# Kernel tuning notes

Measured on AMD Instinct MI355X. Metric: run time of the kernel, lower is better.

## Reference

```python
import jax, jax.numpy as jnp
import numpy as np

N, E = 20000, 320000
IN, HID, HEADS, OUT = 512, 128, 2, 64


def setup_inputs() -> dict:
    key = jax.random.key(0)
    ks = jax.random.split(key, 16)
    g = lambda k, shape, fan: jax.random.normal(k, shape, jnp.float32) * np.float32(1.0 / np.sqrt(fan))
    HC = HEADS * HID
    return {
        "x": jax.random.normal(ks[0], (N, IN), jnp.float32),
        "edge_index": jax.random.randint(ks[1], (2, E), 0, N, dtype=jnp.int32),
        "edge_attr": jax.random.uniform(ks[2], (E, 1), jnp.float32),
        # GATv2Conv 1: lin_l, lin_r (both biased), lin_edge (no bias), att [H,C], out bias [H*C]
        "W1l": g(ks[3], (IN, HC), IN), "b1l": jnp.zeros((HC,), jnp.float32),
        "W1r": g(ks[4], (IN, HC), IN), "b1r": jnp.zeros((HC,), jnp.float32),
        "W1e": g(ks[5], (1, HC), 1), "att1": g(ks[6], (HEADS, HID), HID),
        "bias1": jnp.zeros((HC,), jnp.float32),
        # GATv2Conv 2: heads=1
        "W2l": g(ks[7], (HC, OUT), HC), "b2l": jnp.zeros((OUT,), jnp.float32),
        "W2r": g(ks[8], (HC, OUT), HC), "b2r": jnp.zeros((OUT,), jnp.float32),
        "W2e": g(ks[9], (1, OUT), 1), "att2": g(ks[10], (1, OUT), OUT),
        "bias2": jnp.zeros((OUT,), jnp.float32),
    }


def _gatv2(x, src, dst, eattr, Wl, bl, Wr, br, We, att, bias, H, C):
    """One GATv2Conv layer (edge_dim=1, add_self_loops with fill_value='mean',
    concat=True, negative_slope=0.2, eval mode -> no dropout)."""
    n = x.shape[0]
    xl = (x @ Wl + bl).reshape(n, H, C)  # source-side transform
    xr = (x @ Wr + br).reshape(n, H, C)  # target-side transform
    # self-loop edge_attr = mean of incoming edge attrs per node
    ones = jnp.ones((src.shape[0],), x.dtype)
    deg = jax.ops.segment_sum(ones, dst, num_segments=n)
    loop_attr = jax.ops.segment_sum(eattr, dst, num_segments=n) / jnp.clip(deg, 1.0)[:, None]
    loop = jnp.arange(n, dtype=src.dtype)
    s = jnp.concatenate([src, loop])
    d = jnp.concatenate([dst, loop])
    ea = jnp.concatenate([eattr, loop_attr], axis=0)  # [E+N, 1]
    eemb = (ea @ We).reshape(-1, H, C)
    # per-edge GATv2 score: a^T LeakyReLU(x_l[src] + x_r[dst] + e)
    m = jax.nn.leaky_relu(xl[s] + xr[d] + eemb, 0.2)  # [E+N, H, C]
    alpha = jnp.einsum('ehc,hc->eh', m, att)  # [E+N, H]
    # segment softmax over destination neighborhoods (stable)
    amax = jax.ops.segment_max(alpha, d, num_segments=n)
    ez = jnp.exp(alpha - amax[d])
    denom = jax.ops.segment_sum(ez, d, num_segments=n)
    a = ez / denom[d]
    out = jax.ops.segment_sum(xl[s] * a[:, :, None], d, num_segments=n)  # [n, H, C]
    return out.reshape(n, H * C) + bias


def reference(x, edge_index, edge_attr, W1l, b1l, W1r, b1r, W1e, att1, bias1,
              W2l, b2l, W2r, b2r, W2e, att2, bias2):
    src, dst = edge_index[0], edge_index[1]
    h = _gatv2(x, src, dst, edge_attr, W1l, b1l, W1r, b1r, W1e, att1, bias1, HEADS, HID)
    h = jax.nn.elu(h)
    return _gatv2(h, src, dst, edge_attr, W2l, b2l, W2r, b2r, W2e, att2, bias2, 1, OUT)
```

## Files before the change

kernel.cpp:

```cpp
#include <hip/hip_runtime.h>

#define N_NODES 20000
#define E_EDGES 320000
#define EN_TOT  (E_EDGES + N_NODES)
#define IN_DIM  512
#define H1      2
#define C1      128
#define HC1     256
#define OUT_DIM 64

typedef __attribute__((ext_vector_type(8))) short short8;
typedef __attribute__((ext_vector_type(4))) float f32x4;
typedef __attribute__((ext_vector_type(2))) float f32x2;

__device__ __forceinline__ unsigned short f2bf(float f) {
  unsigned u = __float_as_uint(f);
  u += 0x7fffu + ((u >> 16) & 1u);
  return (unsigned short)(u >> 16);
}
__device__ __forceinline__ float bf2f(unsigned short s) {
  return __uint_as_float(((unsigned)s) << 16);
}
__device__ __forceinline__ f32x2 bfpair(unsigned u) {
  f32x2 r;
  r.x = __uint_as_float(u << 16);
  r.y = __uint_as_float(u & 0xffff0000u);
  return r;
}
__device__ __forceinline__ f32x2 vabs2(f32x2 v) {
  f32x2 r;
  r.x = __uint_as_float(__float_as_uint(v.x) & 0x7fffffffu);
  r.y = __uint_as_float(__float_as_uint(v.y) & 0x7fffffffu);
  return r;
}
__device__ __forceinline__ f32x2 vfma2(f32x2 a, f32x2 b, f32x2 c) {
  return __builtin_elementwise_fma(a, b, c);
}
__device__ __forceinline__ f32x2 vbc2(float s) { f32x2 r; r.x = s; r.y = s; return r; }

#define DPP_XOR1 0xB1
#define DPP_XOR2 0x4E
#define DPP_HM   0x141
#define DPP_M    0x140
template<int CTRL>
__device__ __forceinline__ float dpp_add(float v) {
  return v + __int_as_float(__builtin_amdgcn_update_dpp(
      0, __float_as_int(v), CTRL, 0xF, 0xF, true));
}

__device__ __forceinline__ void gl_lds16(const void* g, void* l) {
  __builtin_amdgcn_global_load_lds((const __attribute__((address_space(1))) void*)g,
                                   (__attribute__((address_space(3))) void*)l, 16, 0, 0);
}

#define STATS_BLOCKS 1250
#define XCONV_BLOCKS 10000
#define PREP_IL (STATS_BLOCKS * 9)
__global__ void prep_kernel(const int* __restrict__ dst, const float* __restrict__ eattr,
                            unsigned long long* __restrict__ pk,
                            const float* __restrict__ x, unsigned short* __restrict__ xb,
                            const float* __restrict__ W1l, const float* __restrict__ W1r,
                            const float* __restrict__ b1l, const float* __restrict__ b1r,
                            unsigned short* __restrict__ W1T, float* __restrict__ bcat1,
                            const float* __restrict__ W2l, const float* __restrict__ W2r,
                            const float* __restrict__ b2l, const float* __restrict__ b2r,
                            unsigned short* __restrict__ W2T, float* __restrict__ bcat2) {
  int bid = blockIdx.x;
  if (bid < PREP_IL) {
    int phase = bid % 9;
    if (phase == 8) {
      int e = (bid / 9) * 256 + threadIdx.x;
      if (e < E_EDGES) {
        int dd = dst[e];
        unsigned long long v = (1ull << 40) |
            (unsigned long long)(unsigned)(eattr[e] * 16777216.0f);
        atomicAdd(&pk[dd], v);
      }
    } else {
      int i = ((bid / 9) * 8 + phase) * 256 + threadIdx.x;
      float4 v = *reinterpret_cast<const float4*>(x + (size_t)i * 4);
      ushort4 o;
      o.x = f2bf(v.x); o.y = f2bf(v.y); o.z = f2bf(v.z); o.w = f2bf(v.w);
      *reinterpret_cast<ushort4*>(xb + (size_t)i * 4) = o;
    }
  } else {
    int idx = (bid - PREP_IL) * 256 + threadIdx.x;
    const int B1 = 512 * 512;
    if (idx < B1) {
      int n = idx >> 9, k = idx & 511;
      const float* W = (n < 256) ? W1l : W1r;
      int nn = n & 255;
      W1T[idx] = f2bf(W[(size_t)k * 256 + nn]);
      if (k == 0) bcat1[n] = (n < 256) ? b1l[nn] : b1r[nn];
    } else if (idx < B1 + 128 * 256) {
      int t = idx - B1;
      int n = t >> 8, k = t & 255;
      const float* W = (n < 64) ? W2l : W2r;
      int nn = n & 63;
      W2T[t] = f2bf(W[(size_t)k * 64 + nn]);
      if (k == 0) bcat2[n] = (n < 64) ? b2l[nn] : b2r[nn];
    }
  }
}

__global__ void scan_kernel(const unsigned long long* __restrict__ pk, int* __restrict__ offs) {
  __shared__ int psum[1024];
  const int T = 1024;
  int tid = threadIdx.x;
  const int per = (N_NODES + T - 1) / T;
  int base = tid * per;
  int s = 0;
  for (int i = 0; i < per; ++i) {
    int n = base + i;
    if (n < N_NODES) s += (int)(pk[n] >> 40) + 1;
  }
  psum[tid] = s;
  __syncthreads();
  for (int off = 1; off < T; off <<= 1) {
    int v = (tid >= off) ? psum[tid - off] : 0;
    __syncthreads();
    psum[tid] += v;
    __syncthreads();
  }
  int run = (tid > 0) ? psum[tid - 1] : 0;
  for (int i = 0; i < per; ++i) {
    int n = base + i;
    if (n < N_NODES) {
      offs[n] = run;
      run += (int)(pk[n] >> 40) + 1;
    }
  }
  if (tid == T - 1) offs[N_NODES] = run;
}

#define CSR_BLOCKS  1329
#define GEMM_BLOCKS 1256
__global__ __launch_bounds__(256) void csr_gemm1_kernel(
    const int* __restrict__ src, const int* __restrict__ dst, const float* __restrict__ eattr,
    const int* __restrict__ offs, unsigned long long* __restrict__ pk,
    int2* __restrict__ csr,
    const unsigned short* __restrict__ A,
    const unsigned short* __restrict__ BT,
    const float* __restrict__ bias, unsigned short* __restrict__ C) {
  constexpr int BK = 64;
  __shared__ short8 AsV[128 * 8];
  __shared__ short8 BsV[64 * 8];
  const int bid = blockIdx.x;
  bool is_gemm;
  int sub;
  if (bid < 2 * GEMM_BLOCKS) { is_gemm = !(bid & 1); sub = bid >> 1; }
  else                       { is_gemm = false; sub = GEMM_BLOCKS + (bid - 2 * GEMM_BLOCKS); }
  if (!is_gemm) {
    int t = sub * 256 + threadIdx.x;
    if (t < N_NODES) {
      unsigned long long v = pk[t];
      float sum = (float)(v & 0xFFFFFFFFFFull) * (1.0f / 16777216.0f);
      int deg = offs[t + 1] - offs[t] - 1;
      float la = sum / fmaxf((float)deg, 1.0f);
      csr[offs[t]] = make_int2(t, __float_as_int(la));
    } else if (t < N_NODES + E_EDGES) {
      int e = t - N_NODES;
      int dd = dst[e];
      unsigned long long old = atomicAdd(&pk[dd], (unsigned long long)(-(1ll << 40)));
      int p = offs[dd] + (int)(old >> 40);
      csr[p] = make_int2(src[e], __float_as_int(eattr[e]));
    }
    return;
  }
  const int g = sub;
  const int bm = (g >> 3) * 128;
  const int bn = (g & 7) * 64;
  constexpr int K = 512, N = 512, M = N_NODES;
  const int tid = threadIdx.x;
  const int lane = tid & 63;
  const int wave = tid >> 6;
  const int wr = wave >> 1, wc = wave & 1;
  const int lrow = lane & 15, lk = lane >> 4;

  f32x4 acc[4][2] = {};

  for (int k0 = 0; k0 < K; k0 += BK) {
#pragma unroll
    for (int i = 0; i < 4; ++i) {
      int c = tid + i * 256;
      int m = c >> 3, kbs = c & 7;
      int kb = kbs ^ (m & 7);
      int gr = bm + m;
      if (gr < M)
        gl_lds16(A + (size_t)gr * K + k0 + kb * 8, &AsV[c]);
    }
#pragma unroll
    for (int i = 0; i < 2; ++i) {
      int c = tid + i * 256;
      int n = c >> 3, kbs = c & 7;
      int kb = kbs ^ (n & 7);
      gl_lds16(BT + (size_t)(bn + n) * K + k0 + kb * 8, &BsV[c]);
    }
    __syncthreads();
#pragma unroll
    for (int ks = 0; ks < 2; ++ks) {
      int kb = ks * 4 + lk;
      short8 a[4], b[2];
#pragma unroll
      for (int mf = 0; mf < 4; ++mf) {
        int r = wr * 64 + mf * 16 + lrow;
        a[mf] = AsV[r * 8 + (kb ^ (r & 7))];
      }
#pragma unroll
      for (int nf = 0; nf < 2; ++nf) {
        int n = wc * 32 + nf * 16 + lrow;
        b[nf] = BsV[n * 8 + (kb ^ (n & 7))];
      }
#pragma unroll
      for (int mf = 0; mf < 4; ++mf)
#pragma unroll
        for (int nf = 0; nf < 2; ++nf)
          acc[mf][nf] = __builtin_amdgcn_mfma_f32_16x16x32_bf16(a[mf], b[nf], acc[mf][nf], 0, 0, 0);
    }
    __syncthreads();
  }
#pragma unroll
  for (int mf = 0; mf < 4; ++mf) {
#pragma unroll
    for (int r = 0; r < 4; ++r) {
      int row = bm + wr * 64 + mf * 16 + (lane >> 4) * 4 + r;
      if (row >= M) continue;
#pragma unroll
      for (int nf = 0; nf < 2; ++nf) {
        int col = bn + wc * 32 + nf * 16 + (lane & 15);
        C[(size_t)row * N + col] = f2bf(acc[mf][nf][r] + bias[col]);
      }
    }
  }
}

template<int BM, int BN>
__global__ __launch_bounds__(256) void gemm_tile_kernel(
    const unsigned short* __restrict__ A,
    const unsigned short* __restrict__ BT,
    const float* __restrict__ bias, unsigned short* __restrict__ C,
    int M, int K, int N) {
  constexpr int BK = 64;
  constexpr int MF = BM / 32;
  constexpr int NF = BN / 32;
  __shared__ short8 AsV[BM * 8];
  __shared__ short8 BsV[BN * 8];
  const int bm = blockIdx.x * BM;
  const int bn = blockIdx.y * BN;
  const int tid = threadIdx.x;
  const int lane = tid & 63;
  const int wave = tid >> 6;
  const int wr = wave >> 1, wc = wave & 1;
  const int lrow = lane & 15, lk = lane >> 4;

  f32x4 acc[MF][NF] = {};

  for (int k0 = 0; k0 < K; k0 += BK) {
#pragma unroll
    for (int i = 0; i < BM / 32; ++i) {
      int c = tid + i * 256;
      int m = c >> 3, kbs = c & 7;
      int kb = kbs ^ (m & 7);
      int gr = bm + m;
      if (gr < M)
        gl_lds16(A + (size_t)gr * K + k0 + kb * 8, &AsV[c]);
    }
#pragma unroll
    for (int i = 0; i < BN / 32; ++i) {
      int c = tid + i * 256;
      int n = c >> 3, kbs = c & 7;
      int kb = kbs ^ (n & 7);
      gl_lds16(BT + (size_t)(bn + n) * K + k0 + kb * 8, &BsV[c]);
    }
    __syncthreads();
#pragma unroll
    for (int ks = 0; ks < 2; ++ks) {
      int kb = ks * 4 + lk;
      short8 a[MF], b[NF];
#pragma unroll
      for (int mf = 0; mf < MF; ++mf) {
        int r = wr * (BM / 2) + mf * 16 + lrow;
        a[mf] = AsV[r * 8 + (kb ^ (r & 7))];
      }
#pragma unroll
      for (int nf = 0; nf < NF; ++nf) {
        int n = wc * (BN / 2) + nf * 16 + lrow;
        b[nf] = BsV[n * 8 + (kb ^ (n & 7))];
      }
#pragma unroll
      for (int mf = 0; mf < MF; ++mf)
#pragma unroll
        for (int nf = 0; nf < NF; ++nf)
          acc[mf][nf] = __builtin_amdgcn_mfma_f32_16x16x32_bf16(a[mf], b[nf], acc[mf][nf], 0, 0, 0);
    }
    __syncthreads();
  }
#pragma unroll
  for (int mf = 0; mf < MF; ++mf) {
#pragma unroll
    for (int r = 0; r < 4; ++r) {
      int row = bm + wr * (BM / 2) + mf * 16 + (lane >> 4) * 4 + r;
      if (row >= M) continue;
#pragma unroll
      for (int nf = 0; nf < NF; ++nf) {
        int col = bn + wc * (BN / 2) + nf * 16 + (lane & 15);
        C[(size_t)row * N + col] = f2bf(acc[mf][nf][r] + bias[col]);
      }
    }
  }
}

__global__ __launch_bounds__(256) void fused1_kernel(
    const int* __restrict__ offs, const int2* __restrict__ csr,
    const unsigned short* __restrict__ xc, const float* __restrict__ We,
    const float* __restrict__ att, const float* __restrict__ bias,
    unsigned short* __restrict__ hout) {
  const int wid = threadIdx.x >> 6, lane = threadIdx.x & 63;
  const int d = blockIdx.x * 4 + wid;
  if (d >= N_NODES) return;
  const int c4 = lane * 4;
  uint2 urr = *reinterpret_cast<const uint2*>(xc + (size_t)d * 512 + 256 + c4);
  const f32x2 xr01 = bfpair(urr.x), xr23 = bfpair(urr.y);
  float4 vef = *reinterpret_cast<const float4*>(We + c4);
  float4 vaf = *reinterpret_cast<const float4*>(att + c4);
  f32x2 ve01; ve01.x = vef.x; ve01.y = vef.y;
  f32x2 ve23; ve23.x = vef.z; ve23.y = vef.w;
  f32x2 c101; c101.x = 0.6f * vaf.x; c101.y = 0.6f * vaf.y;
  f32x2 c123; c123.x = 0.6f * vaf.z; c123.y = 0.6f * vaf.w;
  f32x2 c201; c201.x = 0.4f * vaf.x; c201.y = 0.4f * vaf.y;
  f32x2 c223; c223.x = 0.4f * vaf.z; c223.y = 0.4f * vaf.w;
  const int k0 = offs[d], k1 = offs[d + 1];
  float mmax = -1e30f, den = 0.f;
  f32x2 a01 = {0.f, 0.f}, a23 = {0.f, 0.f};
  for (int kb = k0; kb < k1; kb += 64) {
    const int nk = min(64, k1 - kb);
    int2 ce = make_int2(0, 0);
    if (lane < nk) ce = csr[kb + lane];
    uint2 cur[4];
    float eac[4];
#pragma unroll
    for (int i = 0; i < 4; ++i) {
      int s = __shfl(ce.x, i);
      eac[i] = __int_as_float(__shfl(ce.y, i));
      cur[i] = *reinterpret_cast<const uint2*>(xc + (size_t)s * 512 + c4);
    }
    for (int j = 0; j < nk; j += 4) {
      float p[4];
      f32x2 x01s[4], x23s[4];
#pragma unroll
      for (int i = 0; i < 4; ++i) {
        f32x2 x01 = bfpair(cur[i].x), x23 = bfpair(cur[i].y);
        f32x2 eav = vbc2(eac[i]);
        f32x2 m01 = x01 + vfma2(eav, ve01, xr01);
        f32x2 m23 = x23 + vfma2(eav, ve23, xr23);
        f32x2 t = m01 * c101;
        t = vfma2(vabs2(m01), c201, t);
        t = vfma2(m23, c123, t);
        t = vfma2(vabs2(m23), c223, t);
        p[i] = (j + i < nk) ? (t.x + t.y) : -1e30f;
        x01s[i] = x01; x23s[i] = x23;
      }
      if (j + 4 < nk) {
#pragma unroll
        for (int i = 0; i < 4; ++i) {
          int s = __shfl(ce.x, j + 4 + i);
          eac[i] = __int_as_float(__shfl(ce.y, j + 4 + i));
          cur[i] = *reinterpret_cast<const uint2*>(xc + (size_t)s * 512 + c4);
        }
      }
#pragma unroll
      for (int i = 0; i < 4; ++i) p[i] = dpp_add<DPP_XOR1>(p[i]);
#pragma unroll
      for (int i = 0; i < 4; ++i) p[i] = dpp_add<DPP_XOR2>(p[i]);
#pragma unroll
      for (int i = 0; i < 4; ++i) p[i] = dpp_add<DPP_HM>(p[i]);
#pragma unroll
      for (int i = 0; i < 4; ++i) p[i] = dpp_add<DPP_M>(p[i]);
#pragma unroll
      for (int i = 0; i < 4; ++i) p[i] += __shfl_xor(p[i], 16, 64);
      float nm = fmaxf(mmax, fmaxf(fmaxf(p[0], p[1]), fmaxf(p[2], p[3])));
      float corr = __expf(mmax - nm);
      float w0 = __expf(p[0] - nm), w1 = __expf(p[1] - nm);
      float w2 = __expf(p[2] - nm), w3 = __expf(p[3] - nm);
      mmax = nm;
      den = fmaf(den, corr, (w0 + w1) + (w2 + w3));
      f32x2 corrv = vbc2(corr);
      f32x2 t0 = vbc2(w0) * x01s[0];
      t0 = vfma2(vbc2(w1), x01s[1], t0);
      t0 = vfma2(vbc2(w2), x01s[2], t0);
      t0 = vfma2(vbc2(w3), x01s[3], t0);
      a01 = vfma2(a01, corrv, t0);
      f32x2 t1 = vbc2(w0) * x23s[0];
      t1 = vfma2(vbc2(w1), x23s[1], t1);
      t1 = vfma2(vbc2(w2), x23s[2], t1);
      t1 = vfma2(vbc2(w3), x23s[3], t1);
      a23 = vfma2(a23, corrv, t1);
    }
  }
  float rden = 1.f / den;
  float4 b = *reinterpret_cast<const float4*>(bias + c4);
  float r0 = fmaf(a01.x, rden, b.x); r0 = r0 > 0.f ? r0 : expm1f(r0);
  float r1 = fmaf(a01.y, rden, b.y); r1 = r1 > 0.f ? r1 : expm1f(r1);
  float r2 = fmaf(a23.x, rden, b.z); r2 = r2 > 0.f ? r2 : expm1f(r2);
  float r3 = fmaf(a23.y, rden, b.w); r3 = r3 > 0.f ? r3 : expm1f(r3);
  ushort4 o;
  o.x = f2bf(r0); o.y = f2bf(r1); o.z = f2bf(r2); o.w = f2bf(r3);
  *reinterpret_cast<ushort4*>(hout + (size_t)d * HC1 + c4) = o;
}

__global__ __launch_bounds__(256) void fused2_kernel(
    const int* __restrict__ offs, const int2* __restrict__ csr,
    const unsigned short* __restrict__ xc2, const float* __restrict__ We,
    const float* __restrict__ att, const float* __restrict__ bias,
    float* __restrict__ out) {
  const int wid = threadIdx.x >> 6, lane = threadIdx.x & 63;
  const int d = blockIdx.x * 4 + wid;
  if (d >= N_NODES) return;
  float xr = bf2f(xc2[(size_t)d * 128 + 64 + lane]);
  float ve = We[lane];
  float va = att[lane];
  float cc1 = 0.6f * va, cc2 = 0.4f * va;
  const int k0 = offs[d], k1 = offs[d + 1];
  float mmax = -1e30f, den = 0.f, acc = 0.f;
  for (int kb = k0; kb < k1; kb += 64) {
    const int nk = min(64, k1 - kb);
    int2 ce = make_int2(0, 0);
    if (lane < nk) ce = csr[kb + lane];
    float curx[4], eac[4];
#pragma unroll
    for (int i = 0; i < 4; ++i) {
      int s = __shfl(ce.x, i);
      eac[i] = __int_as_float(__shfl(ce.y, i));
      curx[i] = bf2f(xc2[(size_t)s * 128 + lane]);
    }
    for (int j = 0; j < nk; j += 4) {
      float p[4], xs[4];
#pragma unroll
      for (int i = 0; i < 4; ++i) {
        float x = curx[i];
        float m = x + fmaf(eac[i], ve, xr);
        float pp = fmaf(cc2, fabsf(m), cc1 * m);
        p[i] = (j + i < nk) ? pp : -1e30f;
        xs[i] = x;
      }
      if (j + 4 < nk) {
#pragma unroll
        for (int i = 0; i < 4; ++i) {
          int s = __shfl(ce.x, j + 4 + i);
          eac[i] = __int_as_float(__shfl(ce.y, j + 4 + i));
          curx[i] = bf2f(xc2[(size_t)s * 128 + lane]);
        }
      }
#pragma unroll
      for (int i = 0; i < 4; ++i) p[i] = dpp_add<DPP_XOR1>(p[i]);
#pragma unroll
      for (int i = 0; i < 4; ++i) p[i] = dpp_add<DPP_XOR2>(p[i]);
#pragma unroll
      for (int i = 0; i < 4; ++i) p[i] = dpp_add<DPP_HM>(p[i]);
#pragma unroll
      for (int i = 0; i < 4; ++i) p[i] = dpp_add<DPP_M>(p[i]);
#pragma unroll
      for (int i = 0; i < 4; ++i) p[i] += __shfl_xor(p[i], 16, 64);
#pragma unroll
      for (int i = 0; i < 4; ++i) p[i] += __shfl_xor(p[i], 32, 64);
      float nm = fmaxf(mmax, fmaxf(fmaxf(p[0], p[1]), fmaxf(p[2], p[3])));
      float corr = __expf(mmax - nm);
      float w0 = __expf(p[0] - nm), w1 = __expf(p[1] - nm);
      float w2 = __expf(p[2] - nm), w3 = __expf(p[3] - nm);
      mmax = nm;
      den = fmaf(den, corr, (w0 + w1) + (w2 + w3));
      float t = fmaf(w0, xs[0], fmaf(w1, xs[1], fmaf(w2, xs[2], w3 * xs[3])));
      acc = fmaf(acc, corr, t);
    }
  }
  out[(size_t)d * OUT_DIM + lane] = acc / den + bias[lane];
}

extern "C" void kernel_launch(void* const* d_in, const int* in_sizes, int n_in,
                              void* d_out, int out_size, void* d_ws, size_t ws_size,
                              hipStream_t stream) {
  const float* x     = (const float*)d_in[0];
  const int*   ei    = (const int*)d_in[1];
  const float* eattr = (const float*)d_in[2];
  const float* W1l   = (const float*)d_in[3];
  const float* b1l   = (const float*)d_in[4];
  const float* W1r   = (const float*)d_in[5];
  const float* b1r   = (const float*)d_in[6];
  const float* W1e   = (const float*)d_in[7];
  const float* att1  = (const float*)d_in[8];
  const float* bias1 = (const float*)d_in[9];
  const float* W2l   = (const float*)d_in[10];
  const float* b2l   = (const float*)d_in[11];
  const float* W2r   = (const float*)d_in[12];
  const float* b2r   = (const float*)d_in[13];
  const float* W2e   = (const float*)d_in[14];
  const float* att2  = (const float*)d_in[15];
  const float* bias2 = (const float*)d_in[16];
  const int* src = ei;
  const int* dst = ei + E_EDGES;
  float* out = (float*)d_out;

  char* w = (char*)d_ws;
  unsigned short* xb  = (unsigned short*)w;  w += (size_t)N_NODES * IN_DIM * 2;
  unsigned short* W1T = (unsigned short*)w;  w += (size_t)IN_DIM * 512 * 2;
  unsigned short* W2T = (unsigned short*)w;  w += (size_t)128 * HC1 * 2;
  unsigned short* xc1 = (unsigned short*)w;  w += (size_t)N_NODES * 512 * 2;
  unsigned short* h   = (unsigned short*)w;  w += (size_t)N_NODES * HC1 * 2;
  unsigned short* xc2 = (unsigned short*)w;  w += (size_t)N_NODES * 128 * 2;
  float* bcat1  = (float*)w;                 w += 512 * 4;
  float* bcat2  = (float*)w;                 w += 128 * 4;
  unsigned long long* pk = (unsigned long long*)w;  w += (size_t)N_NODES * 8;
  int* offs     = (int*)w;                   w += (size_t)(N_NODES + 4) * 4;
  int2* csr     = (int2*)w;                  w += (size_t)EN_TOT * 8;

  (void)hipMemsetAsync(pk, 0, (size_t)N_NODES * 8, stream);

  const int T = 256;
  {
    int wprep_blocks = (512 * 512 + 128 * 256 + T - 1) / T;
    prep_kernel<<<PREP_IL + wprep_blocks, T, 0, stream>>>(
        dst, eattr, pk, x, xb, W1l, W1r, b1l, b1r, W1T, bcat1,
        W2l, W2r, b2l, b2r, W2T, bcat2);
  }
  scan_kernel<<<1, 1024, 0, stream>>>(pk, offs);

  csr_gemm1_kernel<<<2 * GEMM_BLOCKS + (CSR_BLOCKS - GEMM_BLOCKS), T, 0, stream>>>(
      src, dst, eattr, offs, pk, csr, xb, W1T, bcat1, xc1);

  fused1_kernel<<<(N_NODES + 3) / 4, T, 0, stream>>>(offs, csr, xc1, W1e, att1, bias1, h);

  {
    dim3 grid((N_NODES + 63) / 64, 128 / 64);
    gemm_tile_kernel<64, 64><<<grid, T, 0, stream>>>(h, W2T, bcat2, xc2, N_NODES, HC1, 128);
  }
  fused2_kernel<<<(N_NODES + 3) / 4, T, 0, stream>>>(offs, csr, xc2, W2e, att2, bias2, out);
}
```

Measured before the change: 163.6 us.

## Widen layer-1 GEMM tiles and split online softmax into two accumulator chains

The fused CSR+GEMM1 kernel now uses 128x128 output tiles instead of 128x64. That halves the number of GEMM blocks and doubles the B-tile reuse per A load, at the cost of more accumulator registers and LDS. Separately, both aggregation kernels alternate between two independent online-softmax accumulators (A/B) per 4-edge group and merge them at the end. This is meant to break the serial max/exp/correction dependency chain. Because the update is chosen by a branch on the group index, the code may not give the intended overlap, and register pressure rises.

Measured after the change: 164.3 us. Within noise of the previous version (+0.4%).

```diff
diff --git a/kernel.cpp b/kernel.cpp
--- a/kernel.cpp
+++ b/kernel.cpp
@@ -134,7 +134,7 @@
 }
 
 #define CSR_BLOCKS  1329
-#define GEMM_BLOCKS 1256
+#define GEMM_BLOCKS 628
 __global__ __launch_bounds__(256) void csr_gemm1_kernel(
     const int* __restrict__ src, const int* __restrict__ dst, const float* __restrict__ eattr,
     const int* __restrict__ offs, unsigned long long* __restrict__ pk,
@@ -144,7 +144,7 @@
     const float* __restrict__ bias, unsigned short* __restrict__ C) {
   constexpr int BK = 64;
   __shared__ short8 AsV[128 * 8];
-  __shared__ short8 BsV[64 * 8];
+  __shared__ short8 BsV[128 * 8];
   const int bid = blockIdx.x;
   bool is_gemm;
   int sub;
@@ -168,8 +168,8 @@
     return;
   }
   const int g = sub;
-  const int bm = (g >> 3) * 128;
-  const int bn = (g & 7) * 64;
+  const int bm = (g >> 2) * 128;
+  const int bn = (g & 3) * 128;
   constexpr int K = 512, N = 512, M = N_NODES;
   const int tid = threadIdx.x;
   const int lane = tid & 63;
@@ -177,7 +177,7 @@
   const int wr = wave >> 1, wc = wave & 1;
   const int lrow = lane & 15, lk = lane >> 4;
 
-  f32x4 acc[4][2] = {};
+  f32x4 acc[4][4] = {};
 
   for (int k0 = 0; k0 < K; k0 += BK) {
 #pragma unroll
@@ -190,7 +190,7 @@
         gl_lds16(A + (size_t)gr * K + k0 + kb * 8, &AsV[c]);
     }
 #pragma unroll
-    for (int i = 0; i < 2; ++i) {
+    for (int i = 0; i < 4; ++i) {
       int c = tid + i * 256;
       int n = c >> 3, kbs = c & 7;
       int kb = kbs ^ (n & 7);
@@ -200,21 +200,21 @@
 #pragma unroll
     for (int ks = 0; ks < 2; ++ks) {
       int kb = ks * 4 + lk;
-      short8 a[4], b[2];
+      short8 a[4], b[4];
 #pragma unroll
       for (int mf = 0; mf < 4; ++mf) {
         int r = wr * 64 + mf * 16 + lrow;
         a[mf] = AsV[r * 8 + (kb ^ (r & 7))];
       }
 #pragma unroll
-      for (int nf = 0; nf < 2; ++nf) {
-        int n = wc * 32 + nf * 16 + lrow;
+      for (int nf = 0; nf < 4; ++nf) {
+        int n = wc * 64 + nf * 16 + lrow;
         b[nf] = BsV[n * 8 + (kb ^ (n & 7))];
       }
 #pragma unroll
       for (int mf = 0; mf < 4; ++mf)
 #pragma unroll
-        for (int nf = 0; nf < 2; ++nf)
+        for (int nf = 0; nf < 4; ++nf)
           acc[mf][nf] = __builtin_amdgcn_mfma_f32_16x16x32_bf16(a[mf], b[nf], acc[mf][nf], 0, 0, 0);
     }
     __syncthreads();
@@ -226,8 +226,8 @@
       int row = bm + wr * 64 + mf * 16 + (lane >> 4) * 4 + r;
       if (row >= M) continue;
 #pragma unroll
-      for (int nf = 0; nf < 2; ++nf) {
-        int col = bn + wc * 32 + nf * 16 + (lane & 15);
+      for (int nf = 0; nf < 4; ++nf) {
+        int col = bn + wc * 64 + nf * 16 + (lane & 15);
         C[(size_t)row * N + col] = f2bf(acc[mf][nf][r] + bias[col]);
       }
     }
@@ -330,8 +330,9 @@
   f32x2 c201; c201.x = 0.4f * vaf.x; c201.y = 0.4f * vaf.y;
   f32x2 c223; c223.x = 0.4f * vaf.z; c223.y = 0.4f * vaf.w;
   const int k0 = offs[d], k1 = offs[d + 1];
-  float mmax = -1e30f, den = 0.f;
-  f32x2 a01 = {0.f, 0.f}, a23 = {0.f, 0.f};
+  float mA = -1e30f, dnA = 0.f, mB = -1e30f, dnB = 0.f;
+  f32x2 aA01 = {0.f, 0.f}, aA23 = {0.f, 0.f};
+  f32x2 aB01 = {0.f, 0.f}, aB23 = {0.f, 0.f};
   for (int kb = k0; kb < k1; kb += 64) {
     const int nk = min(64, k1 - kb);
     int2 ce = make_int2(0, 0);
@@ -378,25 +379,37 @@
       for (int i = 0; i < 4; ++i) p[i] = dpp_add<DPP_M>(p[i]);
 #pragma unroll
       for (int i = 0; i < 4; ++i) p[i] += __shfl_xor(p[i], 16, 64);
-      float nm = fmaxf(mmax, fmaxf(fmaxf(p[0], p[1]), fmaxf(p[2], p[3])));
-      float corr = __expf(mmax - nm);
-      float w0 = __expf(p[0] - nm), w1 = __expf(p[1] - nm);
-      float w2 = __expf(p[2] - nm), w3 = __expf(p[3] - nm);
-      mmax = nm;
-      den = fmaf(den, corr, (w0 + w1) + (w2 + w3));
-      f32x2 corrv = vbc2(corr);
-      f32x2 t0 = vbc2(w0) * x01s[0];
-      t0 = vfma2(vbc2(w1), x01s[1], t0);
-      t0 = vfma2(vbc2(w2), x01s[2], t0);
-      t0 = vfma2(vbc2(w3), x01s[3], t0);
-      a01 = vfma2(a01, corrv, t0);
-      f32x2 t1 = vbc2(w0) * x23s[0];
-      t1 = vfma2(vbc2(w1), x23s[1], t1);
-      t1 = vfma2(vbc2(w2), x23s[2], t1);
-      t1 = vfma2(vbc2(w3), x23s[3], t1);
-      a23 = vfma2(a23, corrv, t1);
-    }
-  }
+      float pmax = fmaxf(fmaxf(p[0], p[1]), fmaxf(p[2], p[3]));
+#define UPDATE1(MM, DN, A01, A23)                                            \
+      {                                                                      \
+        float nm = fmaxf(MM, pmax);                                          \
+        float corr = __expf(MM - nm);                                        \
+        float w0 = __expf(p[0] - nm), w1 = __expf(p[1] - nm);                \
+        float w2 = __expf(p[2] - nm), w3 = __expf(p[3] - nm);                \
+        MM = nm;                                                             \
+        DN = fmaf(DN, corr, (w0 + w1) + (w2 + w3));                          \
+        f32x2 corrv = vbc2(corr);                                            \
+        f32x2 t0 = vbc2(w0) * x01s[0];                                       \
+        t0 = vfma2(vbc2(w1), x01s[1], t0);                                   \
+        t0 = vfma2(vbc2(w2), x01s[2], t0);                                   \
+        t0 = vfma2(vbc2(w3), x01s[3], t0);                                   \
+        A01 = vfma2(A01, corrv, t0);                                         \
+        f32x2 t1 = vbc2(w0) * x23s[0];                                       \
+        t1 = vfma2(vbc2(w1), x23s[1], t1);                                   \
+        t1 = vfma2(vbc2(w2), x23s[2], t1);                                   \
+        t1 = vfma2(vbc2(w3), x23s[3], t1);                                   \
+        A23 = vfma2(A23, corrv, t1);                                         \
+      }
+      if (j & 4) UPDATE1(mB, dnB, aB01, aB23)
+      else       UPDATE1(mA, dnA, aA01, aA23)
+#undef UPDATE1
+    }
+  }
+  float M = fmaxf(mA, mB);
+  float cA = __expf(mA - M), cB = __expf(mB - M);
+  float den = fmaf(dnA, cA, dnB * cB);
+  f32x2 a01 = vfma2(aA01, vbc2(cA), aB01 * vbc2(cB));
+  f32x2 a23 = vfma2(aA23, vbc2(cA), aB23 * vbc2(cB));
   float rden = 1.f / den;
   float4 b = *reinterpret_cast<const float4*>(bias + c4);
   float r0 = fmaf(a01.x, rden, b.x); r0 = r0 > 0.f ? r0 : expm1f(r0);
@@ -421,7 +434,8 @@
   float va = att[lane];
   float cc1 = 0.6f * va, cc2 = 0.4f * va;
   const int k0 = offs[d], k1 = offs[d + 1];
-  float mmax = -1e30f, den = 0.f, acc = 0.f;
+  float mA = -1e30f, dnA = 0.f, accA = 0.f;
+  float mB = -1e30f, dnB = 0.f, accB = 0.f;
   for (int kb = k0; kb < k1; kb += 64) {
     const int nk = min(64, k1 - kb);
     int2 ce = make_int2(0, 0);
@@ -463,16 +477,27 @@
       for (int i = 0; i < 4; ++i) p[i] += __shfl_xor(p[i], 16, 64);
 #pragma unroll
       for (int i = 0; i < 4; ++i) p[i] += __shfl_xor(p[i], 32, 64);
-      float nm = fmaxf(mmax, fmaxf(fmaxf(p[0], p[1]), fmaxf(p[2], p[3])));
-      float corr = __expf(mmax - nm);
-      float w0 = __expf(p[0] - nm), w1 = __expf(p[1] - nm);
-      float w2 = __expf(p[2] - nm), w3 = __expf(p[3] - nm);
-      mmax = nm;
-      den = fmaf(den, corr, (w0 + w1) + (w2 + w3));
-      float t = fmaf(w0, xs[0], fmaf(w1, xs[1], fmaf(w2, xs[2], w3 * xs[3])));
-      acc = fmaf(acc, corr, t);
-    }
-  }
+      float pmax = fmaxf(fmaxf(p[0], p[1]), fmaxf(p[2], p[3]));
+#define UPDATE2(MM, DN, AC)                                                  \
+      {                                                                      \
+        float nm = fmaxf(MM, pmax);                                          \
+        float corr = __expf(MM - nm);                                        \
+        float w0 = __expf(p[0] - nm), w1 = __expf(p[1] - nm);                \
+        float w2 = __expf(p[2] - nm), w3 = __expf(p[3] - nm);                \
+        MM = nm;                                                             \
+        DN = fmaf(DN, corr, (w0 + w1) + (w2 + w3));                          \
+        float t = fmaf(w0, xs[0], fmaf(w1, xs[1], fmaf(w2, xs[2], w3 * xs[3])));\
+        AC = fmaf(AC, corr, t);                                              \
+      }
+      if (j & 4) UPDATE2(mB, dnB, accB)
+      else       UPDATE2(mA, dnA, accA)
+#undef UPDATE2
+    }
+  }
+  float M = fmaxf(mA, mB);
+  float cA = __expf(mA - M), cB = __expf(mB - M);
+  float den = fmaf(dnA, cA, dnB * cB);
+  float acc = fmaf(accA, cA, accB * cB);
   out[(size_t)d * OUT_DIM + lane] = acc / den + bias[lane];
 }
 
```
